# Kernel optimization log

Hardware: AMD Instinct MI355X
Metric: run time of the kernel (lower is better)

## Reference

```python
import jax, jax.numpy as jnp
import numpy as np

H = 8
D = 64
EPS = 1e-5
TEMP = 1.0


def _ln(x, w, b):
    m = jnp.mean(x, axis=-1, keepdims=True)
    v = jnp.var(x, axis=-1, keepdims=True)
    return (x - m) * jax.lax.rsqrt(v + EPS) * w + b


def setup_inputs() -> dict:
    key = jax.random.key(0)
    ks = jax.random.split(key, 8)
    B, T, C = 4, 1024, 512
    x = jax.random.normal(ks[0], (B, T, C), dtype=jnp.float32)
    pair = jax.random.normal(ks[1], (B, T, T, H), dtype=jnp.float32)
    mask = jax.random.randint(ks[2], (B, T, T), 0, 2).astype(bool)
    s = 0.02
    return {
        "x": x,
        "pair": pair,
        "mask": mask,
        "norm_w": jnp.ones((C,), jnp.float32),
        "norm_b": jnp.zeros((C,), jnp.float32),
        "qkv_w": jax.random.normal(ks[3], (3 * C, C), jnp.float32) * s,
        "qkv_b": jnp.zeros((3 * C,), jnp.float32),
        "qln_w": jnp.ones((C,), jnp.float32),
        "qln_b": jnp.zeros((C,), jnp.float32),
        "kln_w": jnp.ones((C,), jnp.float32),
        "kln_b": jnp.zeros((C,), jnp.float32),
        "proj_w": jax.random.normal(ks[4], (C, C), jnp.float32) * s,
        "proj_b": jnp.zeros((C,), jnp.float32),
    }


def reference(x, pair, mask, norm_w, norm_b, qkv_w, qkv_b, qln_w, qln_b,
              kln_w, kln_b, proj_w, proj_b):
    B, T, C = x.shape
    # pre-norm
    xn = _ln(x, norm_w, norm_b)
    qkv = xn @ qkv_w.T + qkv_b  # [B,T,3C]
    q, k, v = jnp.split(qkv, 3, axis=-1)
    q = _ln(q, qln_w, qln_b)
    k = _ln(k, kln_w, kln_b)
    # [B,T,C] -> [B,H,T,D]
    to_heads = lambda t: t.reshape(B, T, H, D).transpose(0, 2, 1, 3)
    q, k, v = to_heads(q), to_heads(k), to_heads(v)
    scale = (D ** -0.5) / TEMP
    sim = jnp.einsum("bhid,bhjd->bhij", q, k) * scale
    sim = sim + pair.transpose(0, 3, 1, 2)  # additive pair bias [B,H,T,T]
    neg = jnp.finfo(sim.dtype).min
    sim = jnp.where(mask[:, None, :, :], sim, sim + neg)
    attn = jax.nn.softmax(sim, axis=-1)
    out = jnp.einsum("bhij,bhjd->bhid", attn, v)
    out = out.transpose(0, 2, 1, 3).reshape(B, T, C)
    return out @ proj_w.T + proj_b
```

## Files before the change

### kernel.cpp

```cpp
#include <hip/hip_runtime.h>
#include <math.h>

#define B_  4
#define T_  1024
#define C_  512
#define H_  8
#define D_  64
#define N3_ 1536
#define BT_ 4096

constexpr float kEps = 1e-5f;
constexpr float kNeg = -3.4028234663852886e38f;
constexpr float kMaskNeg = -1e38f;
constexpr float kShift = 12.0f;

typedef __attribute__((ext_vector_type(8))) short bf16x8;
typedef __attribute__((ext_vector_type(4))) float f32x4;

__device__ __forceinline__ short f2bf(float f) {
  union { float f; unsigned u; } v; v.f = f;
  unsigned r = v.u + 0x7FFFu + ((v.u >> 16) & 1u);
  return (short)(r >> 16);
}
__device__ __forceinline__ float bf2f(unsigned short b) {
  union { unsigned u; float f; } v;
  v.u = ((unsigned)b) << 16;
  return v.f;
}

__device__ __forceinline__ void gld16(const void* g, void* l) {
  __builtin_amdgcn_global_load_lds(
      (const __attribute__((address_space(1))) unsigned int*)g,
      (__attribute__((address_space(3))) unsigned int*)l, 16, 0, 0);
}

__global__ __launch_bounds__(64) void mask_detect_kernel(
    const unsigned int* __restrict__ m, int* __restrict__ flag) {
  int lane = threadIdx.x;
  int any_big = 0;
#pragma unroll
  for (int p = 0; p < 16; ++p) {
    unsigned int v = m[lane + p * 64];
    any_big |= (v > 1u);
  }
  unsigned long long b = __ballot(any_big);
  if (lane == 0) flag[0] = (b != 0ull) ? 1 : 0;
}

__global__ __launch_bounds__(256) void mask_convert_kernel(
    const void* __restrict__ mraw, const int* __restrict__ flag,
    uchar4* __restrict__ out) {
  int idx = blockIdx.x * 256 + threadIdx.x;
  uchar4 v;
  if (flag[0]) {
    v = ((const uchar4*)mraw)[idx];
    v.x = v.x ? 1 : 0; v.y = v.y ? 1 : 0; v.z = v.z ? 1 : 0; v.w = v.w ? 1 : 0;
  } else {
    int4 w = ((const int4*)mraw)[idx];
    v = make_uchar4(w.x != 0, w.y != 0, w.z != 0, w.w != 0);
  }
  out[idx] = v;
}

__global__ __launch_bounds__(256) void pair_prep_kernel(
    const float* __restrict__ pair, const void* __restrict__ mraw,
    short* __restrict__ biast) {
  __shared__ short P[8][1024 + 8];
  unsigned wv = ((const unsigned*)mraw)[threadIdx.x];
  int is_u8 = __syncthreads_or(wv > 1u);
  int bi = blockIdx.x;
  int b = bi >> 10, i = bi & 1023;
  int tid = threadIdx.x;
  const float* src = pair + (size_t)bi * (T_ * H_);
#pragma unroll
  for (int p = 0; p < 8; ++p) {
    int c = tid + p * 256;
    int j = c >> 1, hh = (c & 1) * 4;
    float4 v = *(const float4*)&src[c * 4];
    P[hh + 0][j] = f2bf(v.x);
    P[hh + 1][j] = f2bf(v.y);
    P[hh + 2][j] = f2bf(v.z);
    P[hh + 3][j] = f2bf(v.w);
  }
  bool mk[4];
  if (is_u8) {
    uchar4 mv = ((const uchar4*)mraw)[bi * 256 + tid];
    mk[0] = mv.x; mk[1] = mv.y; mk[2] = mv.z; mk[3] = mv.w;
  } else {
    int4 mv = ((const int4*)mraw)[bi * 256 + tid];
    mk[0] = mv.x != 0; mk[1] = mv.y != 0; mk[2] = mv.z != 0; mk[3] = mv.w != 0;
  }
  __syncthreads();
  const short negb = f2bf(kMaskNeg);
  int j = tid * 4;
#pragma unroll
  for (int h = 0; h < 8; ++h) {
    short4 o;
    o.x = mk[0] ? P[h][j + 0] : negb;
    o.y = mk[1] ? P[h][j + 1] : negb;
    o.z = mk[2] ? P[h][j + 2] : negb;
    o.w = mk[3] ? P[h][j + 3] : negb;
    *(short4*)&biast[((size_t)(b * 8 + h) * T_ + i) * T_ + j] = o;
  }
}

__global__ __launch_bounds__(256) void wcvt2_kernel(
    const float* __restrict__ a, short* __restrict__ oa,
    const float* __restrict__ b, short* __restrict__ ob, int nblk_a) {
  int bid = blockIdx.x;
  const float* src; short* dst; int idx;
  if (bid < nblk_a) { src = a; dst = oa; idx = bid * 256 + threadIdx.x; }
  else             { src = b; dst = ob; idx = (bid - nblk_a) * 256 + threadIdx.x; }
  int i = idx * 4;
  float4 v = *(const float4*)&src[i];
  short4 o;
  o.x = f2bf(v.x); o.y = f2bf(v.y); o.z = f2bf(v.z); o.w = f2bf(v.w);
  *(short4*)&dst[i] = o;
}

__global__ __launch_bounds__(128) void ln_x_kernel(
    const float* __restrict__ x, const float* __restrict__ w,
    const float* __restrict__ b, short* __restrict__ xn) {
  int row = blockIdx.x;
  int tid = threadIdx.x;
  const float* xr = x + (size_t)row * C_;
  float4 v = *(const float4*)&xr[tid * 4];
  float s  = v.x + v.y + v.z + v.w;
  float ss = v.x * v.x + v.y * v.y + v.z * v.z + v.w * v.w;
#pragma unroll
  for (int o = 32; o > 0; o >>= 1) {
    s  += __shfl_down(s, o);
    ss += __shfl_down(ss, o);
  }
  __shared__ float sh[4];
  int wid = tid >> 6, lane = tid & 63;
  if (lane == 0) { sh[wid] = s; sh[2 + wid] = ss; }
  __syncthreads();
  float m   = (sh[0] + sh[1]) * (1.0f / C_);
  float var = (sh[2] + sh[3]) * (1.0f / C_) - m * m;
  float inv = rsqrtf(var + kEps);
  float4 wv = *(const float4*)&w[tid * 4];
  float4 bv = *(const float4*)&b[tid * 4];
  short4 o4;
  o4.x = f2bf((v.x - m) * inv * wv.x + bv.x);
  o4.y = f2bf((v.y - m) * inv * wv.y + bv.y);
  o4.z = f2bf((v.z - m) * inv * wv.z + bv.z);
  o4.w = f2bf((v.w - m) * inv * wv.w + bv.w);
  *(short4*)&xn[(size_t)row * C_ + tid * 4] = o4;
}

__global__ __launch_bounds__(256) void gemm_bf16_kernel(
    const short* __restrict__ A, const short* __restrict__ W,
    const float* __restrict__ bias, float* __restrict__ Cmat,
    int M, int N, int K) {
  __shared__ short As[128 * 64];
  __shared__ short Bs[64 * 64];
  int tid = threadIdx.x;
  int lane = tid & 63, wave = tid >> 6;
  int wm = wave >> 1, wn = wave & 1;
  int col = lane & 15, quad = lane >> 4;
  int m0 = blockIdx.y * 128, n0 = blockIdx.x * 64;
  int wbase = tid & ~63;

  f32x4 acc[4][2];
#pragma unroll
  for (int mi = 0; mi < 4; ++mi)
#pragma unroll
    for (int ni = 0; ni < 2; ++ni) acc[mi][ni] = {0.f, 0.f, 0.f, 0.f};

  for (int k0 = 0; k0 < K; k0 += 64) {
    __syncthreads();
#pragma unroll
    for (int p = 0; p < 4; ++p) {
      int c = tid + p * 256;
      int row = c >> 3, kc = (c & 7) * 8;
      gld16(&A[(size_t)(m0 + row) * K + k0 + kc],
            &As[(wbase + p * 256) * 8]);
    }
#pragma unroll
    for (int p = 0; p < 2; ++p) {
      int c = tid + p * 256;
      int row = c >> 3, kc = (c & 7) * 8;
      gld16(&W[(size_t)(n0 + row) * K + k0 + kc],
            &Bs[(wbase + p * 256) * 8]);
    }
    __syncthreads();
#pragma unroll
    for (int s = 0; s < 2; ++s) {
      bf16x8 af[4], bf[2];
#pragma unroll
      for (int mi = 0; mi < 4; ++mi)
        af[mi] = *(const bf16x8*)&As[(64 * wm + 16 * mi + col) * 64 + s * 32 + quad * 8];
#pragma unroll
      for (int ni = 0; ni < 2; ++ni)
        bf[ni] = *(const bf16x8*)&Bs[(32 * wn + 16 * ni + col) * 64 + s * 32 + quad * 8];
#pragma unroll
      for (int mi = 0; mi < 4; ++mi)
#pragma unroll
        for (int ni = 0; ni < 2; ++ni)
          acc[mi][ni] = __builtin_amdgcn_mfma_f32_16x16x32_bf16(
              af[mi], bf[ni], acc[mi][ni], 0, 0, 0);
    }
  }
#pragma unroll
  for (int ni = 0; ni < 2; ++ni) {
    int n = n0 + 32 * wn + 16 * ni + col;
    float bv = bias[n];
#pragma unroll
    for (int mi = 0; mi < 4; ++mi) {
#pragma unroll
      for (int r = 0; r < 4; ++r) {
        int m = m0 + 64 * wm + 16 * mi + quad * 4 + r;
        Cmat[(size_t)m * N + n] = acc[mi][ni][r] + bv;
      }
    }
  }
}

__global__ __launch_bounds__(128) void qkv_ln_split_kernel(
    const float* __restrict__ qkv,
    const float* __restrict__ qw, const float* __restrict__ qb,
    const float* __restrict__ kw, const float* __restrict__ kb,
    short* __restrict__ qh, short* __restrict__ kh, short* __restrict__ vh) {
  int row = blockIdx.x;
  int b = row >> 10, t = row & 1023;
  int tid = threadIdx.x;
  const float* base = qkv + (size_t)row * N3_;
  int c4 = tid * 4;
  float4 qv = *(const float4*)&base[c4];
  float4 kv = *(const float4*)&base[C_ + c4];
  float4 vv = *(const float4*)&base[2 * C_ + c4];
  float sq  = qv.x + qv.y + qv.z + qv.w;
  float sqq = qv.x * qv.x + qv.y * qv.y + qv.z * qv.z + qv.w * qv.w;
  float sk  = kv.x + kv.y + kv.z + kv.w;
  float skk = kv.x * kv.x + kv.y * kv.y + kv.z * kv.z + kv.w * kv.w;
#pragma unroll
  for (int o = 32; o > 0; o >>= 1) {
    sq  += __shfl_down(sq, o);
    sqq += __shfl_down(sqq, o);
    sk  += __shfl_down(sk, o);
    skk += __shfl_down(skk, o);
  }
  __shared__ float sh[8];
  int wid = tid >> 6, lane = tid & 63;
  if (lane == 0) { sh[wid] = sq; sh[2 + wid] = sqq; sh[4 + wid] = sk; sh[6 + wid] = skk; }
  __syncthreads();
  float qm   = (sh[0] + sh[1]) * (1.0f / C_);
  float qvar = (sh[2] + sh[3]) * (1.0f / C_) - qm * qm;
  float km   = (sh[4] + sh[5]) * (1.0f / C_);
  float kvar = (sh[6] + sh[7]) * (1.0f / C_) - km * km;
  float qi = rsqrtf(qvar + kEps);
  float ki = rsqrtf(kvar + kEps);
  float4 qwv = *(const float4*)&qw[c4];
  float4 qbv = *(const float4*)&qb[c4];
  float4 kwv = *(const float4*)&kw[c4];
  float4 kbv = *(const float4*)&kb[c4];
  int h = tid >> 4;
  int d = (tid & 15) * 4;
  size_t dst = ((size_t)(b * H_ + h) * T_ + t) * D_ + d;
  short4 qo, ko, vo;
  qo.x = f2bf(((qv.x - qm) * qi * qwv.x + qbv.x) * 0.125f);
  qo.y = f2bf(((qv.y - qm) * qi * qwv.y + qbv.y) * 0.125f);
  qo.z = f2bf(((qv.z - qm) * qi * qwv.z + qbv.z) * 0.125f);
  qo.w = f2bf(((qv.w - qm) * qi * qwv.w + qbv.w) * 0.125f);
  ko.x = f2bf((kv.x - km) * ki * kwv.x + kbv.x);
  ko.y = f2bf((kv.y - km) * ki * kwv.y + kbv.y);
  ko.z = f2bf((kv.z - km) * ki * kwv.z + kbv.z);
  ko.w = f2bf((kv.w - km) * ki * kwv.w + kbv.w);
  vo.x = f2bf(vv.x); vo.y = f2bf(vv.y); vo.z = f2bf(vv.z); vo.w = f2bf(vv.w);
  *(short4*)&qh[dst] = qo;
  *(short4*)&kh[dst] = ko;
  *(short4*)&vh[dst] = vo;
}

__global__ __launch_bounds__(256) void attn_split_kernel(
    const short* __restrict__ qh, const short* __restrict__ kh,
    const short* __restrict__ vh, const short* __restrict__ biast,
    float* __restrict__ Opart, float* __restrict__ lpart) {
  __shared__ short Ks[64 * 72];
  __shared__ short Vt[64 * 72];
  __shared__ short Ps[64 * 72];
  int tid = threadIdx.x;
  int lane = tid & 63, w = tid >> 6;
  int col = lane & 15, quad = lane >> 4;
  int bh = blockIdx.y;
  int half = blockIdx.z;
  int i0 = blockIdx.x * 64;
  const short* Qg = qh + (size_t)bh * T_ * D_;
  const short* Kg = kh + (size_t)bh * T_ * D_;
  const short* Vg = vh + (size_t)bh * T_ * D_;
  const unsigned short* Bpu =
      (const unsigned short*)(biast + (size_t)bh * T_ * T_);

  bf16x8 qf[2];
#pragma unroll
  for (int s = 0; s < 2; ++s)
    qf[s] = *(const bf16x8*)&Qg[(size_t)(i0 + 16 * w + col) * D_ + s * 32 + quad * 8];

  float lsum[4];
  f32x4 oacc[4];
#pragma unroll
  for (int r = 0; r < 4; ++r) lsum[r] = 0.f;
#pragma unroll
  for (int dt = 0; dt < 4; ++dt) oacc[dt] = {0.f, 0.f, 0.f, 0.f};

  int jbase = half * (T_ / 2);
  for (int jj = 0; jj < T_ / 2; jj += 64) {
    int j0 = jbase + jj;
    __syncthreads();
#pragma unroll
    for (int p = 0; p < 2; ++p) {
      int c = tid + p * 256;
      int row = c >> 3, dc = (c & 7) * 8;
      *(int4*)&Ks[row * 72 + dc] =
          *(const int4*)&Kg[(size_t)(j0 + row) * D_ + dc];
    }
    {
      int j = tid & 63, d0 = (tid >> 6) * 16;
#pragma unroll
      for (int p = 0; p < 2; ++p) {
        short tmp[8];
        *(int4*)tmp = *(const int4*)&Vg[(size_t)(j0 + j) * D_ + d0 + p * 8];
#pragma unroll
        for (int q = 0; q < 8; ++q) Vt[(d0 + p * 8 + q) * 72 + j] = tmp[q];
      }
    }
    __syncthreads();

    unsigned short bsv[4][4];
#pragma unroll
    for (int r = 0; r < 4; ++r) {
      int gi = i0 + 16 * w + quad * 4 + r;
#pragma unroll
      for (int jt = 0; jt < 4; ++jt)
        bsv[r][jt] = Bpu[(size_t)gi * T_ + j0 + 16 * jt + col];
    }

    f32x4 sacc[4];
#pragma unroll
    for (int jt = 0; jt < 4; ++jt) sacc[jt] = {0.f, 0.f, 0.f, 0.f};
#pragma unroll
    for (int s = 0; s < 2; ++s) {
#pragma unroll
      for (int jt = 0; jt < 4; ++jt) {
        bf16x8 kf = *(const bf16x8*)&Ks[(16 * jt + col) * 72 + s * 32 + quad * 8];
        sacc[jt] = __builtin_amdgcn_mfma_f32_16x16x32_bf16(qf[s], kf, sacc[jt], 0, 0, 0);
      }
    }

#pragma unroll
    for (int r = 0; r < 4; ++r) {
      int li = 16 * w + quad * 4 + r;
#pragma unroll
      for (int jt = 0; jt < 4; ++jt) {
        float s = sacc[jt][r] + bf2f(bsv[r][jt]);
        float p = __expf(fminf(s - kShift, 60.0f));
        lsum[r] += p;
        Ps[li * 72 + 16 * jt + col] = f2bf(p);
      }
    }
    __syncthreads();

#pragma unroll
    for (int s = 0; s < 2; ++s) {
      bf16x8 pf = *(const bf16x8*)&Ps[(16 * w + col) * 72 + s * 32 + quad * 8];
#pragma unroll
      for (int dt = 0; dt < 4; ++dt) {
        bf16x8 vf = *(const bf16x8*)&Vt[(16 * dt + col) * 72 + s * 32 + quad * 8];
        oacc[dt] = __builtin_amdgcn_mfma_f32_16x16x32_bf16(pf, vf, oacc[dt], 0, 0, 0);
      }
    }
  }

#pragma unroll
  for (int r = 0; r < 4; ++r) {
    float l = lsum[r];
#pragma unroll
    for (int o = 1; o < 16; o <<= 1) l += __shfl_xor(l, o);
    int gi = i0 + 16 * w + quad * 4 + r;
    size_t orow = (size_t)half * 32768 + (size_t)bh * T_ + gi;
    if (col == 0) lpart[orow] = l;
#pragma unroll
    for (int dt = 0; dt < 4; ++dt)
      Opart[orow * 64 + 16 * dt + col] = oacc[dt][r];
  }
}

__global__ __launch_bounds__(256) void attn_merge_kernel(
    const float* __restrict__ Opart, const float* __restrict__ lpart,
    short* __restrict__ ao) {
  int g = blockIdx.x * 256 + threadIdx.x;
  int row = g >> 4, d4 = (g & 15) * 4;
  float4 o0 = *(const float4*)&Opart[(size_t)row * 64 + d4];
  float4 o1 = *(const float4*)&Opart[((size_t)32768 + row) * 64 + d4];
  float inv = 1.0f / (lpart[row] + lpart[32768 + row]);
  int bh = row >> 10, gi = row & 1023;
  int b = bh >> 3, h = bh & 7;
  short4 o;
  o.x = f2bf((o0.x + o1.x) * inv);
  o.y = f2bf((o0.y + o1.y) * inv);
  o.z = f2bf((o0.z + o1.z) * inv);
  o.w = f2bf((o0.w + o1.w) * inv);
  *(short4*)&ao[((size_t)(b * T_ + gi)) * C_ + h * D_ + d4] = o;
}

__global__ __launch_bounds__(256) void attn_kernel(
    const short* __restrict__ qh, const short* __restrict__ kh,
    const short* __restrict__ vh, const float* __restrict__ pair,
    const unsigned char* __restrict__ mask, short* __restrict__ ao) {
  __shared__ short Ks[64 * 72];
  __shared__ short Vt[64 * 72];
  __shared__ short Ps[64 * 72];
  int tid = threadIdx.x;
  int lane = tid & 63, w = tid >> 6;
  int col = lane & 15, quad = lane >> 4;
  int bh = blockIdx.y;
  int b = bh >> 3, h = bh & 7;
  int i0 = blockIdx.x * 64;
  const short* Qg = qh + (size_t)bh * T_ * D_;
  const short* Kg = kh + (size_t)bh * T_ * D_;
  const short* Vg = vh + (size_t)bh * T_ * D_;

  bf16x8 qf[2];
#pragma unroll
  for (int s = 0; s < 2; ++s)
    qf[s] = *(const bf16x8*)&Qg[(size_t)(i0 + 16 * w + col) * D_ + s * 32 + quad * 8];

  float mrun[4], lrun[4];
  f32x4 oacc[4];
#pragma unroll
  for (int r = 0; r < 4; ++r) { mrun[r] = -INFINITY; lrun[r] = 0.f; }
#pragma unroll
  for (int dt = 0; dt < 4; ++dt) oacc[dt] = {0.f, 0.f, 0.f, 0.f};

  for (int j0 = 0; j0 < T_; j0 += 64) {
    __syncthreads();
#pragma unroll
    for (int p = 0; p < 2; ++p) {
      int c = tid + p * 256;
      int row = c >> 3, dc = (c & 7) * 8;
      *(int4*)&Ks[row * 72 + dc] =
          *(const int4*)&Kg[(size_t)(j0 + row) * D_ + dc];
    }
    {
      int j = tid & 63, d0 = (tid >> 6) * 16;
#pragma unroll
      for (int p = 0; p < 2; ++p) {
        short tmp[8];
        *(int4*)tmp = *(const int4*)&Vg[(size_t)(j0 + j) * D_ + d0 + p * 8];
#pragma unroll
        for (int q = 0; q < 8; ++q) Vt[(d0 + p * 8 + q) * 72 + j] = tmp[q];
      }
    }
    __syncthreads();

    f32x4 sacc[4];
#pragma unroll
    for (int jt = 0; jt < 4; ++jt) sacc[jt] = {0.f, 0.f, 0.f, 0.f};
#pragma unroll
    for (int s = 0; s < 2; ++s) {
#pragma unroll
      for (int jt = 0; jt < 4; ++jt) {
        bf16x8 kf = *(const bf16x8*)&Ks[(16 * jt + col) * 72 + s * 32 + quad * 8];
        sacc[jt] = __builtin_amdgcn_mfma_f32_16x16x32_bf16(qf[s], kf, sacc[jt], 0, 0, 0);
      }
    }

#pragma unroll
    for (int r = 0; r < 4; ++r) {
      int gi = i0 + 16 * w + quad * 4 + r;
      const float* prow = pair + (size_t)(b * T_ + gi) * (T_ * H_) + h;
      const unsigned char* mrow = mask + (size_t)(b * T_ + gi) * T_;
      float sv[4];
      float rm = -INFINITY;
#pragma unroll
      for (int jt = 0; jt < 4; ++jt) {
        int j = j0 + 16 * jt + col;
        float s = sacc[jt][r] + prow[(size_t)j * H_];
        if (!mrow[j]) s += kNeg;
        sv[jt] = s;
        rm = fmaxf(rm, s);
      }
#pragma unroll
      for (int o = 8; o > 0; o >>= 1) rm = fmaxf(rm, __shfl_xor(rm, o));
      float mnew  = fmaxf(mrun[r], rm);
      float alpha = __expf(mrun[r] - mnew);
      float psum = 0.f;
#pragma unroll
      for (int jt = 0; jt < 4; ++jt) {
        float p = __expf(sv[jt] - mnew);
        psum += p;
        Ps[(16 * w + quad * 4 + r) * 72 + 16 * jt + col] = f2bf(p);
      }
#pragma unroll
      for (int o = 8; o > 0; o >>= 1) psum += __shfl_xor(psum, o);
      lrun[r] = lrun[r] * alpha + psum;
      mrun[r] = mnew;
#pragma unroll
      for (int dt = 0; dt < 4; ++dt) oacc[dt][r] *= alpha;
    }
    __syncthreads();

#pragma unroll
    for (int s = 0; s < 2; ++s) {
      bf16x8 pf = *(const bf16x8*)&Ps[(16 * w + col) * 72 + s * 32 + quad * 8];
#pragma unroll
      for (int dt = 0; dt < 4; ++dt) {
        bf16x8 vf = *(const bf16x8*)&Vt[(16 * dt + col) * 72 + s * 32 + quad * 8];
        oacc[dt] = __builtin_amdgcn_mfma_f32_16x16x32_bf16(pf, vf, oacc[dt], 0, 0, 0);
      }
    }
  }

#pragma unroll
  for (int r = 0; r < 4; ++r) {
    int gi = i0 + 16 * w + quad * 4 + r;
    float inv = 1.0f / lrun[r];
    size_t base = (size_t)(b * T_ + gi) * C_ + h * D_;
#pragma unroll
    for (int dt = 0; dt < 4; ++dt)
      ao[base + 16 * dt + col] = f2bf(oacc[dt][r] * inv);
  }
}

extern "C" void kernel_launch(void* const* d_in, const int* in_sizes, int n_in,
                              void* d_out, int out_size, void* d_ws, size_t ws_size,
                              hipStream_t stream) {
  const float* x      = (const float*)d_in[0];
  const float* pair   = (const float*)d_in[1];
  const void*  maskraw = d_in[2];
  const float* norm_w = (const float*)d_in[3];
  const float* norm_b = (const float*)d_in[4];
  const float* qkv_w  = (const float*)d_in[5];
  const float* qkv_b  = (const float*)d_in[6];
  const float* qln_w  = (const float*)d_in[7];
  const float* qln_b  = (const float*)d_in[8];
  const float* kln_w  = (const float*)d_in[9];
  const float* kln_b  = (const float*)d_in[10];
  const float* proj_w = (const float*)d_in[11];
  const float* proj_b = (const float*)d_in[12];
  float* out = (float*)d_out;

  short* xn = (short*)d_out;
  short* qh = (short*)d_out + (size_t)BT_ * C_;

  const size_t MB = 1024 * 1024;

  if (ws_size >= 96 * MB) {
    char* base = (char*)d_ws;
    short* biast = (short*)base;
    float* qkv   = (float*)base;
    float* Opart = (float*)(base + 64 * MB);
    float* lpart = (float*)(base + 80 * MB);
    short* ao    = (short*)(base + 81 * MB);
    short* kh    = (short*)(base + 85 * MB);
    short* vh    = (short*)(base + 89 * MB);
    short* wq    = (short*)(base + 93 * MB);
    short* wp    = (short*)(base + 94 * MB + 512 * 1024);

    wcvt2_kernel<<<(N3_ * C_ + C_ * C_) / 1024, 256, 0, stream>>>(
        qkv_w, wq, proj_w, wp, (N3_ * C_) / 1024);
    ln_x_kernel<<<BT_, 128, 0, stream>>>(x, norm_w, norm_b, xn);
    gemm_bf16_kernel<<<dim3(N3_ / 64, BT_ / 128), 256, 0, stream>>>(
        xn, wq, qkv_b, qkv, BT_, N3_, C_);
    qkv_ln_split_kernel<<<BT_, 128, 0, stream>>>(
        qkv, qln_w, qln_b, kln_w, kln_b, qh, kh, vh);
    pair_prep_kernel<<<B_ * T_, 256, 0, stream>>>(pair, maskraw, biast);
    attn_split_kernel<<<dim3(T_ / 64, B_ * H_, 2), 256, 0, stream>>>(
        qh, kh, vh, biast, Opart, lpart);
    attn_merge_kernel<<<2048, 256, 0, stream>>>(Opart, lpart, ao);
    gemm_bf16_kernel<<<dim3(C_ / 64, BT_ / 128), 256, 0, stream>>>(
        ao, wp, proj_b, out, BT_, C_, C_);
  } else {
    float* qkv = (float*)d_ws;
    short* ao  = (short*)d_ws;
    short* sw  = (short*)d_ws;
    short* wq  = sw + (size_t)12 * 1024 * 1024;
    short* wp  = wq + (size_t)N3_ * C_;
    short* kh  = sw + (size_t)13 * 1024 * 1024;
    short* vh  = sw + (size_t)15 * 1024 * 1024;
    unsigned char* maskc = (unsigned char*)d_ws + (size_t)34 * MB;
    int* flag = (int*)((unsigned char*)d_ws + (size_t)38 * MB);

    mask_detect_kernel<<<1, 64, 0, stream>>>((const unsigned int*)maskraw, flag);
    mask_convert_kernel<<<(B_ * T_ * T_) / 1024, 256, 0, stream>>>(
        maskraw, flag, (uchar4*)maskc);
    wcvt2_kernel<<<(N3_ * C_ + C_ * C_) / 1024, 256, 0, stream>>>(
        qkv_w, wq, proj_w, wp, (N3_ * C_) / 1024);
    ln_x_kernel<<<BT_, 128, 0, stream>>>(x, norm_w, norm_b, xn);
    gemm_bf16_kernel<<<dim3(N3_ / 64, BT_ / 128), 256, 0, stream>>>(
        xn, wq, qkv_b, qkv, BT_, N3_, C_);
    qkv_ln_split_kernel<<<BT_, 128, 0, stream>>>(
        qkv, qln_w, qln_b, kln_w, kln_b, qh, kh, vh);
    attn_kernel<<<dim3(T_ / 64, B_ * H_), 256, 0, stream>>>(
        qh, kh, vh, pair, maskc, ao);
    gemm_bf16_kernel<<<dim3(C_ / 64, BT_ / 128), 256, 0, stream>>>(
        ao, wp, proj_b, out, BT_, C_, C_);
  }
}
```

Baseline: 308.1 us.

## Enlarge attention query tile, use exp2 with prescaled bias, widen QKV GEMM tile

The split attention kernel now runs 512 threads over 128 query rows per block, so each K/V tile loaded into shared memory serves twice as many rows. The bias loads are issued before the barrier, and the barrier between writing P and the PV MFMA is dropped because each wave only reads its own P rows. Softmax switches to exp2 with the pair bias prescaled by log2(e) in pair_prep. The QKV projection uses a new 128x128-tile GEMM for more reuse per block. The risks are fewer resident blocks and lower occupancy from the larger blocks, and slightly different rounding from the prescaled bias.

```diff
diff --git a/kernel.cpp b/kernel.cpp
--- a/kernel.cpp
+++ b/kernel.cpp
@@ -11,8 +11,9 @@
 
 constexpr float kEps = 1e-5f;
 constexpr float kNeg = -3.4028234663852886e38f;
-constexpr float kMaskNeg = -1e38f;
-constexpr float kShift = 12.0f;
+constexpr float kMaskNeg = -1.4e38f;
+constexpr float kLog2e = 1.44269504088896f;
+constexpr float kShift2 = 17.312340490667562f;
 
 typedef __attribute__((ext_vector_type(8))) short bf16x8;
 typedef __attribute__((ext_vector_type(4))) float f32x4;
@@ -77,10 +78,10 @@
     int c = tid + p * 256;
     int j = c >> 1, hh = (c & 1) * 4;
     float4 v = *(const float4*)&src[c * 4];
-    P[hh + 0][j] = f2bf(v.x);
-    P[hh + 1][j] = f2bf(v.y);
-    P[hh + 2][j] = f2bf(v.z);
-    P[hh + 3][j] = f2bf(v.w);
+    P[hh + 0][j] = f2bf(v.x * kLog2e);
+    P[hh + 1][j] = f2bf(v.y * kLog2e);
+    P[hh + 2][j] = f2bf(v.z * kLog2e);
+    P[hh + 3][j] = f2bf(v.w * kLog2e);
   }
   bool mk[4];
   if (is_u8) {
@@ -149,6 +150,72 @@
   *(short4*)&xn[(size_t)row * C_ + tid * 4] = o4;
 }
 
+__global__ __launch_bounds__(256) void gemm_bf16_128_kernel(
+    const short* __restrict__ A, const short* __restrict__ W,
+    const float* __restrict__ bias, float* __restrict__ Cmat,
+    int M, int N, int K) {
+  __shared__ short As[128 * 64];
+  __shared__ short Bs[128 * 64];
+  int tid = threadIdx.x;
+  int lane = tid & 63, wave = tid >> 6;
+  int wm = wave >> 1, wn = wave & 1;
+  int col = lane & 15, quad = lane >> 4;
+  int m0 = blockIdx.y * 128, n0 = blockIdx.x * 128;
+  int wbase = tid & ~63;
+
+  f32x4 acc[4][4];
+#pragma unroll
+  for (int mi = 0; mi < 4; ++mi)
+#pragma unroll
+    for (int ni = 0; ni < 4; ++ni) acc[mi][ni] = {0.f, 0.f, 0.f, 0.f};
+
+  for (int k0 = 0; k0 < K; k0 += 64) {
+    __syncthreads();
+#pragma unroll
+    for (int p = 0; p < 4; ++p) {
+      int c = tid + p * 256;
+      int row = c >> 3, kc = (c & 7) * 8;
+      gld16(&A[(size_t)(m0 + row) * K + k0 + kc], &As[(wbase + p * 256) * 8]);
+    }
+#pragma unroll
+    for (int p = 0; p < 4; ++p) {
+      int c = tid + p * 256;
+      int row = c >> 3, kc = (c & 7) * 8;
+      gld16(&W[(size_t)(n0 + row) * K + k0 + kc], &Bs[(wbase + p * 256) * 8]);
+    }
+    __syncthreads();
+#pragma unroll
+    for (int s = 0; s < 2; ++s) {
+      bf16x8 af[4], bfv[4];
+#pragma unroll
+      for (int mi = 0; mi < 4; ++mi)
+        af[mi] = *(const bf16x8*)&As[(64 * wm + 16 * mi + col) * 64 + s * 32 + quad * 8];
+#pragma unroll
+      for (int ni = 0; ni < 4; ++ni)
+        bfv[ni] = *(const bf16x8*)&Bs[(64 * wn + 16 * ni + col) * 64 + s * 32 + quad * 8];
+#pragma unroll
+      for (int mi = 0; mi < 4; ++mi)
+#pragma unroll
+        for (int ni = 0; ni < 4; ++ni)
+          acc[mi][ni] = __builtin_amdgcn_mfma_f32_16x16x32_bf16(
+              af[mi], bfv[ni], acc[mi][ni], 0, 0, 0);
+    }
+  }
+#pragma unroll
+  for (int ni = 0; ni < 4; ++ni) {
+    int n = n0 + 64 * wn + 16 * ni + col;
+    float bv = bias[n];
+#pragma unroll
+    for (int mi = 0; mi < 4; ++mi) {
+#pragma unroll
+      for (int r = 0; r < 4; ++r) {
+        int m = m0 + 64 * wm + 16 * mi + quad * 4 + r;
+        Cmat[(size_t)m * N + n] = acc[mi][ni][r] + bv;
+      }
+    }
+  }
+}
+
 __global__ __launch_bounds__(256) void gemm_bf16_kernel(
     const short* __restrict__ A, const short* __restrict__ W,
     const float* __restrict__ bias, float* __restrict__ Cmat,
@@ -174,32 +241,30 @@
     for (int p = 0; p < 4; ++p) {
       int c = tid + p * 256;
       int row = c >> 3, kc = (c & 7) * 8;
-      gld16(&A[(size_t)(m0 + row) * K + k0 + kc],
-            &As[(wbase + p * 256) * 8]);
+      gld16(&A[(size_t)(m0 + row) * K + k0 + kc], &As[(wbase + p * 256) * 8]);
     }
 #pragma unroll
     for (int p = 0; p < 2; ++p) {
       int c = tid + p * 256;
       int row = c >> 3, kc = (c & 7) * 8;
-      gld16(&W[(size_t)(n0 + row) * K + k0 + kc],
-            &Bs[(wbase + p * 256) * 8]);
+      gld16(&W[(size_t)(n0 + row) * K + k0 + kc], &Bs[(wbase + p * 256) * 8]);
     }
     __syncthreads();
 #pragma unroll
     for (int s = 0; s < 2; ++s) {
-      bf16x8 af[4], bf[2];
+      bf16x8 af[4], bfv[2];
 #pragma unroll
       for (int mi = 0; mi < 4; ++mi)
         af[mi] = *(const bf16x8*)&As[(64 * wm + 16 * mi + col) * 64 + s * 32 + quad * 8];
 #pragma unroll
       for (int ni = 0; ni < 2; ++ni)
-        bf[ni] = *(const bf16x8*)&Bs[(32 * wn + 16 * ni + col) * 64 + s * 32 + quad * 8];
+        bfv[ni] = *(const bf16x8*)&Bs[(32 * wn + 16 * ni + col) * 64 + s * 32 + quad * 8];
 #pragma unroll
       for (int mi = 0; mi < 4; ++mi)
 #pragma unroll
         for (int ni = 0; ni < 2; ++ni)
           acc[mi][ni] = __builtin_amdgcn_mfma_f32_16x16x32_bf16(
-              af[mi], bf[ni], acc[mi][ni], 0, 0, 0);
+              af[mi], bfv[ni], acc[mi][ni], 0, 0, 0);
     }
   }
 #pragma unroll
@@ -273,19 +338,19 @@
   *(short4*)&vh[dst] = vo;
 }
 
-__global__ __launch_bounds__(256) void attn_split_kernel(
+__global__ __launch_bounds__(512, 4) void attn_split_kernel(
     const short* __restrict__ qh, const short* __restrict__ kh,
     const short* __restrict__ vh, const short* __restrict__ biast,
     float* __restrict__ Opart, float* __restrict__ lpart) {
   __shared__ short Ks[64 * 72];
   __shared__ short Vt[64 * 72];
-  __shared__ short Ps[64 * 72];
+  __shared__ short Ps[128 * 72];
   int tid = threadIdx.x;
   int lane = tid & 63, w = tid >> 6;
   int col = lane & 15, quad = lane >> 4;
   int bh = blockIdx.y;
   int half = blockIdx.z;
-  int i0 = blockIdx.x * 64;
+  int i0 = blockIdx.x * 128;
   const short* Qg = qh + (size_t)bh * T_ * D_;
   const short* Kg = kh + (size_t)bh * T_ * D_;
   const short* Vg = vh + (size_t)bh * T_ * D_;
@@ -307,34 +372,30 @@
   int jbase = half * (T_ / 2);
   for (int jj = 0; jj < T_ / 2; jj += 64) {
     int j0 = jbase + jj;
-    __syncthreads();
-#pragma unroll
-    for (int p = 0; p < 2; ++p) {
-      int c = tid + p * 256;
-      int row = c >> 3, dc = (c & 7) * 8;
+
+    unsigned short bsv[4][4];
+#pragma unroll
+    for (int r = 0; r < 4; ++r) {
+      int gi = i0 + 16 * w + quad * 4 + r;
+#pragma unroll
+      for (int jt = 0; jt < 4; ++jt)
+        bsv[r][jt] = Bpu[(size_t)gi * T_ + j0 + 16 * jt + col];
+    }
+
+    __syncthreads();
+    {
+      int row = tid >> 3, dc = (tid & 7) * 8;
       *(int4*)&Ks[row * 72 + dc] =
           *(const int4*)&Kg[(size_t)(j0 + row) * D_ + dc];
     }
     {
-      int j = tid & 63, d0 = (tid >> 6) * 16;
-#pragma unroll
-      for (int p = 0; p < 2; ++p) {
-        short tmp[8];
-        *(int4*)tmp = *(const int4*)&Vg[(size_t)(j0 + j) * D_ + d0 + p * 8];
-#pragma unroll
-        for (int q = 0; q < 8; ++q) Vt[(d0 + p * 8 + q) * 72 + j] = tmp[q];
-      }
-    }
-    __syncthreads();
-
-    unsigned short bsv[4][4];
-#pragma unroll
-    for (int r = 0; r < 4; ++r) {
-      int gi = i0 + 16 * w + quad * 4 + r;
-#pragma unroll
-      for (int jt = 0; jt < 4; ++jt)
-        bsv[r][jt] = Bpu[(size_t)gi * T_ + j0 + 16 * jt + col];
-    }
+      int j = tid & 63, d0 = (tid >> 6) * 8;
+      short tmp[8];
+      *(int4*)tmp = *(const int4*)&Vg[(size_t)(j0 + j) * D_ + d0];
+#pragma unroll
+      for (int q = 0; q < 8; ++q) Vt[(d0 + q) * 72 + j] = tmp[q];
+    }
+    __syncthreads();
 
     f32x4 sacc[4];
 #pragma unroll
@@ -353,13 +414,12 @@
       int li = 16 * w + quad * 4 + r;
 #pragma unroll
       for (int jt = 0; jt < 4; ++jt) {
-        float s = sacc[jt][r] + bf2f(bsv[r][jt]);
-        float p = __expf(fminf(s - kShift, 60.0f));
+        float sv = fmaf(sacc[jt][r], kLog2e, bf2f(bsv[r][jt]));
+        float p = exp2f(fminf(sv - kShift2, 86.5f));
         lsum[r] += p;
         Ps[li * 72 + 16 * jt + col] = f2bf(p);
       }
     }
-    __syncthreads();
 
 #pragma unroll
     for (int s = 0; s < 2; ++s) {
@@ -561,12 +621,12 @@
     wcvt2_kernel<<<(N3_ * C_ + C_ * C_) / 1024, 256, 0, stream>>>(
         qkv_w, wq, proj_w, wp, (N3_ * C_) / 1024);
     ln_x_kernel<<<BT_, 128, 0, stream>>>(x, norm_w, norm_b, xn);
-    gemm_bf16_kernel<<<dim3(N3_ / 64, BT_ / 128), 256, 0, stream>>>(
+    gemm_bf16_128_kernel<<<dim3(N3_ / 128, BT_ / 128), 256, 0, stream>>>(
         xn, wq, qkv_b, qkv, BT_, N3_, C_);
     qkv_ln_split_kernel<<<BT_, 128, 0, stream>>>(
         qkv, qln_w, qln_b, kln_w, kln_b, qh, kh, vh);
     pair_prep_kernel<<<B_ * T_, 256, 0, stream>>>(pair, maskraw, biast);
-    attn_split_kernel<<<dim3(T_ / 64, B_ * H_, 2), 256, 0, stream>>>(
+    attn_split_kernel<<<dim3(T_ / 128, B_ * H_, 2), 512, 0, stream>>>(
         qh, kh, vh, biast, Opart, lpart);
     attn_merge_kernel<<<2048, 256, 0, stream>>>(Opart, lpart, ao);
     gemm_bf16_kernel<<<dim3(C_ / 64, BT_ / 128), 256, 0, stream>>>(
@@ -588,7 +648,7 @@
     wcvt2_kernel<<<(N3_ * C_ + C_ * C_) / 1024, 256, 0, stream>>>(
         qkv_w, wq, proj_w, wp, (N3_ * C_) / 1024);
     ln_x_kernel<<<BT_, 128, 0, stream>>>(x, norm_w, norm_b, xn);
-    gemm_bf16_kernel<<<dim3(N3_ / 64, BT_ / 128), 256, 0, stream>>>(
+    gemm_bf16_128_kernel<<<dim3(N3_ / 128, BT_ / 128), 256, 0, stream>>>(
         xn, wq, qkv_b, qkv, BT_, N3_, C_);
     qkv_ln_split_kernel<<<BT_, 128, 0, stream>>>(
         qkv, qln_w, qln_b, kln_w, kln_b, qh, kh, vh);
```

New measurement: 316.0 us. +2.6%, slower.
